# Optimization experiments

Hardware: AMD Instinct MI355X
Metric: run time of the kernel (lower is better)

The kernel has to match this reference:

```python
import jax, jax.numpy as jnp
import numpy as np

N_NODES = 100000
N_EDGES = 1600000
N_GRAPHS = 64


def setup_inputs() -> dict:
    key = jax.random.key(0)
    ks = jax.random.split(key, 12)
    x = jax.random.normal(ks[0], (N_NODES, 3), dtype=jnp.float32)
    edge_index = jax.random.randint(ks[1], (2, N_EDGES), 0, N_NODES)
    edge_attr = jax.random.uniform(ks[2], (N_EDGES,), dtype=jnp.float32)
    batch = jnp.sort(jax.random.randint(ks[3], (N_NODES,), 0, N_GRAPHS))

    def glorot(k, shape):
        lim = float(np.sqrt(6.0 / (shape[0] + shape[1])))
        return jax.random.uniform(k, shape, jnp.float32, -lim, lim)

    W1 = glorot(ks[4], (3, 100));    b1 = jnp.zeros((100,), jnp.float32)
    W2 = glorot(ks[5], (100, 200));  b2 = jnp.zeros((200,), jnp.float32)
    Wl1 = glorot(ks[6], (200, 100)); bl1 = jnp.zeros((100,), jnp.float32)
    Wl2 = glorot(ks[7], (100, 1));   bl2 = jnp.zeros((1,), jnp.float32)
    return {"x": x, "edge_attr": edge_attr, "W1": W1, "b1": b1, "W2": W2,
            "b2": b2, "Wl1": Wl1, "bl1": bl1, "Wl2": Wl2, "bl2": bl2,
            "edge_index": edge_index, "batch": batch}


def gcn_conv(x, edge_index, edge_weight, W, b):
    # PyG GCNConv: linear transform, add self-loops (weight 1), symmetric
    # deg^{-1/2} normalization, scatter-add messages source->target, + bias.
    h = x @ W                                   # [N, out]
    n = h.shape[0]
    loops = jnp.arange(n)
    row = jnp.concatenate([edge_index[0], loops])   # sources
    col = jnp.concatenate([edge_index[1], loops])   # targets
    w = jnp.concatenate([edge_weight, jnp.ones((n,), edge_weight.dtype)])
    deg = jax.ops.segment_sum(w, col, num_segments=n)
    dinv = jnp.where(deg > 0, jax.lax.rsqrt(deg), jnp.zeros_like(deg))
    norm = dinv[row] * w * dinv[col]                # [E+N]
    out = jax.ops.segment_sum(norm[:, None] * h[row], col, num_segments=n)
    return out + b


def reference(x, edge_attr, W1, b1, W2, b2, Wl1, bl1, Wl2, bl2, edge_index, batch):
    h = jax.nn.silu(gcn_conv(x, edge_index, edge_attr, W1, b1))
    h = jax.nn.silu(gcn_conv(h, edge_index, edge_attr, W2, b2))
    # global_mean_pool over graphs in the batch
    sums = jax.ops.segment_sum(h, batch, num_segments=N_GRAPHS)
    counts = jax.ops.segment_sum(jnp.ones((h.shape[0],), h.dtype), batch,
                                 num_segments=N_GRAPHS)
    pooled = sums / jnp.maximum(counts, 1.0)[:, None]   # [G, 200]
    h = jax.nn.silu(pooled @ Wl1 + bl1)
    out = h @ Wl2 + bl2                                  # [G, 1]
    return out.squeeze()
```

## Files before the change

kernel.cpp:

```cpp
#include <hip/hip_runtime.h>

#define NN 100000
#define NE 1600000
#define NG 64
#define CAP 64
#define NPB 80
#define NBUCK 391
#define NBLK 391
#define EPB 4096
#define BCAP 4608
#define NSLOT 32

__device__ __forceinline__ float silu_f(float x) { return x / (1.0f + __expf(-x)); }

__global__ void k_scatter(const int* __restrict__ row, const int* __restrict__ col,
                          const float* __restrict__ ew, int* __restrict__ gcnt,
                          int2* __restrict__ sorted, float* __restrict__ pooled2) {
  __shared__ int h[NBUCK];
  __shared__ int base[NBUCK];
  __shared__ int curh[NBUCK];
  int tid = threadIdx.x;
  for (int i = tid; i < NBUCK; i += 512) { h[i] = 0; curh[i] = 0; }
  for (int i = blockIdx.x * 512 + tid; i < NG * NSLOT * 200; i += NBLK * 512)
    pooled2[i] = 0.0f;
  __syncthreads();
  int s = blockIdx.x * EPB;
  for (int i = 0; i < EPB / 2048; ++i) {
    int e = s + i * 2048 + tid * 4;
    if (e + 3 < NE) {
      int4 c4 = *(const int4*)(col + e);
      atomicAdd(&h[c4.x >> 8], 1);
      atomicAdd(&h[c4.y >> 8], 1);
      atomicAdd(&h[c4.z >> 8], 1);
      atomicAdd(&h[c4.w >> 8], 1);
    } else {
      for (int j = 0; j < 4; ++j) {
        int ee = e + j;
        if (ee < NE) atomicAdd(&h[col[ee] >> 8], 1);
      }
    }
  }
  __syncthreads();
  for (int i = tid; i < NBUCK; i += 512)
    base[i] = (h[i] > 0) ? atomicAdd(&gcnt[i * 16], h[i]) : 0;
  __syncthreads();
  for (int i = 0; i < EPB / 2048; ++i) {
    int e = s + i * 2048 + tid * 4;
    if (e + 3 < NE) {
      int4 r4 = *(const int4*)(row + e);
      int4 c4 = *(const int4*)(col + e);
      float4 w4 = *(const float4*)(ew + e);
#define SC1(cc, rr, ww) { \
  int b = (cc) >> 8; \
  int p = base[b] + atomicAdd(&curh[b], 1); \
  if (p < BCAP) \
    sorted[(size_t)b * BCAP + p] = \
        make_int2((rr) | (((cc) & 255) << 17), __float_as_int(ww)); }
      SC1(c4.x, r4.x, w4.x)
      SC1(c4.y, r4.y, w4.y)
      SC1(c4.z, r4.z, w4.z)
      SC1(c4.w, r4.w, w4.w)
    } else {
      for (int j = 0; j < 4; ++j) {
        int ee = e + j;
        if (ee < NE) { SC1(col[ee], row[ee], ew[ee]) }
      }
#undef SC1
    }
  }
}

__global__ void k_group(const int* __restrict__ gcnt, const int2* __restrict__ sorted,
                        int* __restrict__ cur, int2* __restrict__ buck,
                        float* __restrict__ dinv, const float* __restrict__ x,
                        float* __restrict__ y) {
  __shared__ int cnt[256];
  __shared__ float wsum[256];
  int b = blockIdx.x, tid = threadIdx.x;
  int n = min(gcnt[b * 16], BCAP);
  size_t s = (size_t)b * BCAP;
  if (tid < 256) { cnt[tid] = 0; wsum[tid] = 0.0f; }
  __syncthreads();
  for (int i = tid; i < n; i += 512) {
    int2 pk = sorted[s + i];
    int node = (pk.x >> 17) & 255;
    int rank = atomicAdd(&cnt[node], 1);
    atomicAdd(&wsum[node], __int_as_float(pk.y));
    if (rank < CAP)
      buck[(((size_t)b * 256 + node) << 6) + rank] = make_int2(pk.x & 0x1FFFF, pk.y);
  }
  __syncthreads();
  if (tid < 256) {
    int gnode = b * 256 + tid;
    if (gnode < NN) {
      cur[gnode] = cnt[tid];
      float di = rsqrtf(wsum[tid] + 1.0f);
      dinv[gnode] = di;
      y[3 * gnode + 0] = di * x[3 * gnode + 0];
      y[3 * gnode + 1] = di * x[3 * gnode + 1];
      y[3 * gnode + 2] = di * x[3 * gnode + 2];
    }
  }
}

__global__ void k_agg1z(const int* __restrict__ cur, const int2* __restrict__ buck,
                        const float* __restrict__ dinv, const float* __restrict__ y,
                        const float* __restrict__ W1, const float* __restrict__ b1,
                        float* __restrict__ z1p) {
  int wave = threadIdx.x >> 6, lane = threadIdx.x & 63;
  int sub = lane >> 4, rank = lane & 15;
  int cbase = blockIdx.x * 16 + wave * 4;
  int c = cbase + sub;
  int cnt = min(cur[c], CAP);
  float dc = dinv[c];
  float s0 = 0.0f, s1 = 0.0f, s2 = 0.0f;
  for (int p = rank; p < cnt; p += 16) {
    int2 pk = buck[((size_t)c << 6) + p];
    int r = pk.x;
    float ww = __int_as_float(pk.y);
    s0 += ww * y[3 * r + 0];
    s1 += ww * y[3 * r + 1];
    s2 += ww * y[3 * r + 2];
  }
  for (int s = 8; s; s >>= 1) {
    s0 += __shfl_down(s0, s, 16);
    s1 += __shfl_down(s1, s, 16);
    s2 += __shfl_down(s2, s, 16);
  }
  if (rank == 0) {
    s0 = (s0 + y[3 * c + 0]) * dc;
    s1 = (s1 + y[3 * c + 1]) * dc;
    s2 = (s2 + y[3 * c + 2]) * dc;
  }
  float2 w0, w1, w2, bq;
  if (lane < 50) {
    w0 = ((const float2*)(W1))[lane];
    w1 = ((const float2*)(W1 + 100))[lane];
    w2 = ((const float2*)(W1 + 200))[lane];
    bq = ((const float2*)b1)[lane];
  }
#pragma unroll
  for (int n = 0; n < 4; ++n) {
    float t0 = __shfl(s0, n * 16, 64);
    float t1 = __shfl(s1, n * 16, 64);
    float t2 = __shfl(s2, n * 16, 64);
    float dn = __shfl(dc, n * 16, 64);
    if (lane < 50) {
      float2 o;
      o.x = dn * silu_f(bq.x + t0 * w0.x + t1 * w1.x + t2 * w2.x);
      o.y = dn * silu_f(bq.y + t0 * w0.y + t1 * w1.y + t2 * w2.y);
      ((float2*)(z1p + (size_t)(cbase + n) * 100))[lane] = o;
    }
  }
}

__global__ void k_agg2(const float* __restrict__ z1p, const float* __restrict__ dinv,
                       const int* __restrict__ cur, const int2* __restrict__ buck,
                       float* __restrict__ a2) {
  int wave = threadIdx.x >> 6;
  int lane = threadIdx.x & 63;
  int c = blockIdx.x * 4 + wave;
  if (c >= NN) return;
  int grp = lane >> 5;
  int li = lane & 31;
  bool act = li < 25;
  float dc = dinv[c];
  const float4* zv = (const float4*)z1p;
  float4 acc = make_float4(0.f, 0.f, 0.f, 0.f);
  if (grp == 0 && act) {
    float4 v = zv[(size_t)c * 25 + li];
    acc.x = dc * v.x; acc.y = dc * v.y; acc.z = dc * v.z; acc.w = dc * v.w;
  }
  int cnt = min(cur[c], CAP);
  int2 pk = make_int2(0, 0);
  if (lane < cnt) pk = buck[((size_t)c << 6) + lane];
  int p = 0;
#define GATH(off, rv, cv) \
  int rv = __shfl(pk.x, p + (off) + grp, 64); \
  float cv = __int_as_float(__shfl(pk.y, p + (off) + grp, 64)) * dc;
#define ACC(rv, cv) { \
  float4 v = zv[(size_t)rv * 25 + li]; \
  acc.x += cv * v.x; acc.y += cv * v.y; acc.z += cv * v.z; acc.w += cv * v.w; }
  for (; p + 8 <= cnt; p += 8) {
    GATH(0, r0, c0) GATH(2, r1, c1) GATH(4, r2, c2) GATH(6, r3, c3)
    if (act) { ACC(r0, c0) ACC(r1, c1) ACC(r2, c2) ACC(r3, c3) }
  }
  for (; p + 2 <= cnt; p += 2) {
    GATH(0, r0, c0)
    if (act) ACC(r0, c0)
  }
  if (p < cnt) {
    int r0 = __shfl(pk.x, p, 64);
    float c0 = __int_as_float(__shfl(pk.y, p, 64)) * dc;
    if (grp == 0 && act) ACC(r0, c0)
  }
#undef GATH
#undef ACC
  acc.x += __shfl(acc.x, lane + 32, 64);
  acc.y += __shfl(acc.y, lane + 32, 64);
  acc.z += __shfl(acc.z, lane + 32, 64);
  acc.w += __shfl(acc.w, lane + 32, 64);
  if (grp == 0 && act) ((float4*)a2)[(size_t)c * 25 + li] = acc;
}

__global__ void k_h2pool(const float* __restrict__ a2, const float* __restrict__ W2,
                         const float* __restrict__ b2, const int* __restrict__ batch,
                         float* __restrict__ pooled2) {
  __shared__ float zst[100 * 84];
  __shared__ float part[6 * 200];
  __shared__ int bsm[NPB];
  int tid = threadIdx.x;
  int nb = blockIdx.x * NPB;
  int slot = blockIdx.x & (NSLOT - 1);
  const float4* a2v = (const float4*)(a2 + (size_t)nb * 100);
  for (int i = tid; i < NPB * 25; i += 256) {
    int n = i / 25, c = i % 25;
    float4 v = a2v[i];
    zst[(4 * c + 0) * 84 + n] = v.x;
    zst[(4 * c + 1) * 84 + n] = v.y;
    zst[(4 * c + 2) * 84 + n] = v.z;
    zst[(4 * c + 3) * 84 + n] = v.w;
  }
  if (tid < NPB) bsm[tid] = batch[nb + tid];
  for (int i = tid; i < 1200; i += 256) part[i] = 0.0f;
  __syncthreads();
  int gmin = bsm[0];
  int ngr = bsm[NPB - 1] - gmin + 1;
  int q = tid % 25;
  int r = tid / 25;
  if (r < 10) {
    int n0 = r * 8;
    float4 acc0[8], acc1[8];
#pragma unroll
    for (int i = 0; i < 8; ++i) {
      acc0[i] = make_float4(0.f, 0.f, 0.f, 0.f);
      acc1[i] = make_float4(0.f, 0.f, 0.f, 0.f);
    }
    const float4* W2v = (const float4*)W2;
#pragma unroll 2
    for (int k = 0; k < 100; ++k) {
      float4 w0 = W2v[k * 50 + 2 * q];
      float4 w1 = W2v[k * 50 + 2 * q + 1];
      float4 za = *(const float4*)&zst[k * 84 + n0];
      float4 zb = *(const float4*)&zst[k * 84 + n0 + 4];
#define FMA8(ai, zv) \
  acc0[ai].x += (zv) * w0.x; acc0[ai].y += (zv) * w0.y; \
  acc0[ai].z += (zv) * w0.z; acc0[ai].w += (zv) * w0.w; \
  acc1[ai].x += (zv) * w1.x; acc1[ai].y += (zv) * w1.y; \
  acc1[ai].z += (zv) * w1.z; acc1[ai].w += (zv) * w1.w;
      FMA8(0, za.x) FMA8(1, za.y) FMA8(2, za.z) FMA8(3, za.w)
      FMA8(4, zb.x) FMA8(5, zb.y) FMA8(6, zb.z) FMA8(7, zb.w)
#undef FMA8
    }
    float4 b0v = ((const float4*)b2)[2 * q];
    float4 b1v = ((const float4*)b2)[2 * q + 1];
    float4 run0 = make_float4(0.f, 0.f, 0.f, 0.f);
    float4 run1 = make_float4(0.f, 0.f, 0.f, 0.f);
    int curg = bsm[n0];
#define FLUSH(gv) { \
  int gl = (gv) - gmin; \
  if (gl < 6) { \
    float* pr = &part[gl * 200 + 8 * q]; \
    atomicAdd(&pr[0], run0.x); atomicAdd(&pr[1], run0.y); \
    atomicAdd(&pr[2], run0.z); atomicAdd(&pr[3], run0.w); \
    atomicAdd(&pr[4], run1.x); atomicAdd(&pr[5], run1.y); \
    atomicAdd(&pr[6], run1.z); atomicAdd(&pr[7], run1.w); \
  } else { \
    float* pr = &pooled2[((size_t)(gv) * NSLOT + slot) * 200 + 8 * q]; \
    atomicAdd(&pr[0], run0.x); atomicAdd(&pr[1], run0.y); \
    atomicAdd(&pr[2], run0.z); atomicAdd(&pr[3], run0.w); \
    atomicAdd(&pr[4], run1.x); atomicAdd(&pr[5], run1.y); \
    atomicAdd(&pr[6], run1.z); atomicAdd(&pr[7], run1.w); \
  } }
#pragma unroll
    for (int i = 0; i < 8; ++i) {
      float4 s0, s1;
      s0.x = silu_f(acc0[i].x + b0v.x); s0.y = silu_f(acc0[i].y + b0v.y);
      s0.z = silu_f(acc0[i].z + b0v.z); s0.w = silu_f(acc0[i].w + b0v.w);
      s1.x = silu_f(acc1[i].x + b1v.x); s1.y = silu_f(acc1[i].y + b1v.y);
      s1.z = silu_f(acc1[i].z + b1v.z); s1.w = silu_f(acc1[i].w + b1v.w);
      int g = bsm[n0 + i];
      if (g != curg) {
        FLUSH(curg)
        run0 = make_float4(0.f, 0.f, 0.f, 0.f);
        run1 = make_float4(0.f, 0.f, 0.f, 0.f);
        curg = g;
      }
      run0.x += s0.x; run0.y += s0.y; run0.z += s0.z; run0.w += s0.w;
      run1.x += s1.x; run1.y += s1.y; run1.z += s1.z; run1.w += s1.w;
    }
    FLUSH(curg)
#undef FLUSH
  }
  __syncthreads();
  if (tid < 200) {
    int nloop = min(ngr, 6);
    for (int g = 0; g < nloop; ++g)
      pooled2[((size_t)(gmin + g) * NSLOT + slot) * 200 + tid] = part[g * 200 + tid];
  }
}

__global__ void k_final(const float* __restrict__ pooled2, const int* __restrict__ batch,
                        const float* __restrict__ Wl1, const float* __restrict__ bl1,
                        const float* __restrict__ Wl2, const float* __restrict__ bl2,
                        float* __restrict__ out) {
  __shared__ float pm[200];
  __shared__ float hid[100];
  __shared__ int bounds[2];
  int g = blockIdx.x;
  int j = threadIdx.x;
  if (j < 2) {
    int target = g + j;
    int lo = 0, hi = NN;
    while (lo < hi) {
      int mid = (lo + hi) >> 1;
      if (batch[mid] < target) lo = mid + 1; else hi = mid;
    }
    bounds[j] = lo;
  }
  float acc = 0.0f;
  if (j < 200) {
    const float* base = pooled2 + (size_t)g * NSLOT * 200 + j;
    for (int s = 0; s < NSLOT; ++s) acc += base[s * 200];
  }
  __syncthreads();
  int cntg = bounds[1] - bounds[0];
  float inv = 1.0f / (float)((cntg > 0) ? cntg : 1);
  if (j < 200) pm[j] = acc * inv;
  __syncthreads();
  if (j < 100) {
    float a = bl1[j];
    for (int k = 0; k < 200; ++k) a += pm[k] * Wl1[k * 100 + j];
    a = silu_f(a);
    hid[j] = a * Wl2[j];
  }
  __syncthreads();
  if (j == 0) {
    float sum = bl2[0];
    for (int k = 0; k < 100; ++k) sum += hid[k];
    out[g] = sum;
  }
}

extern "C" void kernel_launch(void* const* d_in, const int* in_sizes, int n_in,
                              void* d_out, int out_size, void* d_ws, size_t ws_size,
                              hipStream_t stream) {
  const float* x   = (const float*)d_in[0];
  const float* ew  = (const float*)d_in[1];
  const float* W1  = (const float*)d_in[2];
  const float* b1  = (const float*)d_in[3];
  const float* W2  = (const float*)d_in[4];
  const float* b2  = (const float*)d_in[5];
  const float* Wl1 = (const float*)d_in[6];
  const float* bl1 = (const float*)d_in[7];
  const float* Wl2 = (const float*)d_in[8];
  const float* bl2 = (const float*)d_in[9];
  const int* ei    = (const int*)d_in[10];
  const int* batch = (const int*)d_in[11];
  const int* rowp = ei;
  const int* colp = ei + NE;
  float* out = (float*)d_out;

  char* w = (char*)d_ws;
  size_t o = 0;
  auto alloc = [&](size_t bytes) {
    char* p = w + o;
    o = (o + bytes + 255) & ~(size_t)255;
    return p;
  };
  int*   cur     = (int*)alloc((size_t)NN * 4);
  float* dinv    = (float*)alloc((size_t)NN * 4);
  float* y       = (float*)alloc((size_t)NN * 3 * 4);
  float* pooled2 = (float*)alloc((size_t)NG * NSLOT * 200 * 4);
  float* z1p     = (float*)alloc((size_t)NN * 100 * 4);
  float* a2      = (float*)alloc((size_t)NN * 100 * 4);
  int2*  buck    = (int2*)alloc((size_t)NN * CAP * 8);
  int2*  sorted  = (int2*)alloc((size_t)NBUCK * BCAP * 8);
  int*   gcnt    = (int*)alloc((size_t)NBUCK * 16 * 4);

  hipMemsetAsync(gcnt, 0, (size_t)NBUCK * 16 * 4, stream);

  k_scatter<<<NBLK, 512, 0, stream>>>(rowp, colp, ew, gcnt, sorted, pooled2);
  k_group<<<NBUCK, 512, 0, stream>>>(gcnt, sorted, cur, buck, dinv, x, y);
  k_agg1z<<<NN / 16, 256, 0, stream>>>(cur, buck, dinv, y, W1, b1, z1p);
  k_agg2<<<(NN + 3) / 4, 256, 0, stream>>>(z1p, dinv, cur, buck, a2);
  k_h2pool<<<NN / NPB, 256, 0, stream>>>(a2, W2, b2, batch, pooled2);
  k_final<<<NG, 256, 0, stream>>>(pooled2, batch, Wl1, bl1, Wl2, bl2, out);
}
```

Before: 340.6 us.

## Recompute layer-1 features per edge from 3-wide aggregates instead of gathering 100-wide rows

Layer-1 output is no longer materialised as a 100-float-per-node array. k_agg1 stores only the normalised 3-component aggregate plus dinv in a float4. k_agg2r then recomputes the W1 transform and silu for each gathered neighbor before accumulating. This replaces the 400-byte-per-edge gathers and the large intermediate write with 16-byte gathers, at the cost of about 100 exponentials and FMAs per edge and the loss of the 8-way unrolled gather loop.

```diff
diff --git a/kernel.cpp b/kernel.cpp
--- a/kernel.cpp
+++ b/kernel.cpp
@@ -72,8 +72,7 @@
 
 __global__ void k_group(const int* __restrict__ gcnt, const int2* __restrict__ sorted,
                         int* __restrict__ cur, int2* __restrict__ buck,
-                        float* __restrict__ dinv, const float* __restrict__ x,
-                        float* __restrict__ y) {
+                        const float* __restrict__ x, float4* __restrict__ y4) {
   __shared__ int cnt[256];
   __shared__ float wsum[256];
   int b = blockIdx.x, tid = threadIdx.x;
@@ -95,32 +94,27 @@
     if (gnode < NN) {
       cur[gnode] = cnt[tid];
       float di = rsqrtf(wsum[tid] + 1.0f);
-      dinv[gnode] = di;
-      y[3 * gnode + 0] = di * x[3 * gnode + 0];
-      y[3 * gnode + 1] = di * x[3 * gnode + 1];
-      y[3 * gnode + 2] = di * x[3 * gnode + 2];
-    }
-  }
-}
-
-__global__ void k_agg1z(const int* __restrict__ cur, const int2* __restrict__ buck,
-                        const float* __restrict__ dinv, const float* __restrict__ y,
-                        const float* __restrict__ W1, const float* __restrict__ b1,
-                        float* __restrict__ z1p) {
+      y4[gnode] = make_float4(di * x[3 * gnode + 0], di * x[3 * gnode + 1],
+                              di * x[3 * gnode + 2], di);
+    }
+  }
+}
+
+__global__ void k_agg1(const int* __restrict__ cur, const int2* __restrict__ buck,
+                       const float4* __restrict__ y4, float4* __restrict__ a1d) {
   int wave = threadIdx.x >> 6, lane = threadIdx.x & 63;
   int sub = lane >> 4, rank = lane & 15;
   int cbase = blockIdx.x * 16 + wave * 4;
   int c = cbase + sub;
   int cnt = min(cur[c], CAP);
-  float dc = dinv[c];
   float s0 = 0.0f, s1 = 0.0f, s2 = 0.0f;
   for (int p = rank; p < cnt; p += 16) {
     int2 pk = buck[((size_t)c << 6) + p];
-    int r = pk.x;
     float ww = __int_as_float(pk.y);
-    s0 += ww * y[3 * r + 0];
-    s1 += ww * y[3 * r + 1];
-    s2 += ww * y[3 * r + 2];
+    float4 v = y4[pk.x];
+    s0 += ww * v.x;
+    s1 += ww * v.y;
+    s2 += ww * v.z;
   }
   for (int s = 8; s; s >>= 1) {
     s0 += __shfl_down(s0, s, 16);
@@ -128,35 +122,15 @@
     s2 += __shfl_down(s2, s, 16);
   }
   if (rank == 0) {
-    s0 = (s0 + y[3 * c + 0]) * dc;
-    s1 = (s1 + y[3 * c + 1]) * dc;
-    s2 = (s2 + y[3 * c + 2]) * dc;
-  }
-  float2 w0, w1, w2, bq;
-  if (lane < 50) {
-    w0 = ((const float2*)(W1))[lane];
-    w1 = ((const float2*)(W1 + 100))[lane];
-    w2 = ((const float2*)(W1 + 200))[lane];
-    bq = ((const float2*)b1)[lane];
-  }
-#pragma unroll
-  for (int n = 0; n < 4; ++n) {
-    float t0 = __shfl(s0, n * 16, 64);
-    float t1 = __shfl(s1, n * 16, 64);
-    float t2 = __shfl(s2, n * 16, 64);
-    float dn = __shfl(dc, n * 16, 64);
-    if (lane < 50) {
-      float2 o;
-      o.x = dn * silu_f(bq.x + t0 * w0.x + t1 * w1.x + t2 * w2.x);
-      o.y = dn * silu_f(bq.y + t0 * w0.y + t1 * w1.y + t2 * w2.y);
-      ((float2*)(z1p + (size_t)(cbase + n) * 100))[lane] = o;
-    }
-  }
-}
-
-__global__ void k_agg2(const float* __restrict__ z1p, const float* __restrict__ dinv,
-                       const int* __restrict__ cur, const int2* __restrict__ buck,
-                       float* __restrict__ a2) {
+    float4 vc = y4[c];
+    float dc = vc.w;
+    a1d[c] = make_float4((s0 + vc.x) * dc, (s1 + vc.y) * dc, (s2 + vc.z) * dc, dc);
+  }
+}
+
+__global__ void k_agg2r(const float4* __restrict__ a1d, const int* __restrict__ cur,
+                        const int2* __restrict__ buck, const float* __restrict__ W1,
+                        const float* __restrict__ b1, float* __restrict__ a2) {
   int wave = threadIdx.x >> 6;
   int lane = threadIdx.x & 63;
   int c = blockIdx.x * 4 + wave;
@@ -164,38 +138,44 @@
   int grp = lane >> 5;
   int li = lane & 31;
   bool act = li < 25;
-  float dc = dinv[c];
-  const float4* zv = (const float4*)z1p;
+  float4 w0, w1, w2, bb;
+  if (act) {
+    w0 = ((const float4*)W1)[li];
+    w1 = ((const float4*)(W1 + 100))[li];
+    w2 = ((const float4*)(W1 + 200))[li];
+    bb = ((const float4*)b1)[li];
+  }
+  float4 ac = a1d[c];
+  float dc = ac.w;
   float4 acc = make_float4(0.f, 0.f, 0.f, 0.f);
-  if (grp == 0 && act) {
-    float4 v = zv[(size_t)c * 25 + li];
-    acc.x = dc * v.x; acc.y = dc * v.y; acc.z = dc * v.z; acc.w = dc * v.w;
-  }
+#define ZACC(av, cf) { \
+  float m = (cf) * (av).w; \
+  float vx = bb.x + (av).x * w0.x + (av).y * w1.x + (av).z * w2.x; \
+  float vy = bb.y + (av).x * w0.y + (av).y * w1.y + (av).z * w2.y; \
+  float vz = bb.z + (av).x * w0.z + (av).y * w1.z + (av).z * w2.z; \
+  float vw = bb.w + (av).x * w0.w + (av).y * w1.w + (av).z * w2.w; \
+  acc.x += m * (vx / (1.0f + __expf(-vx))); \
+  acc.y += m * (vy / (1.0f + __expf(-vy))); \
+  acc.z += m * (vz / (1.0f + __expf(-vz))); \
+  acc.w += m * (vw / (1.0f + __expf(-vw))); }
+  if (grp == 0 && act) ZACC(ac, dc)
   int cnt = min(cur[c], CAP);
   int2 pk = make_int2(0, 0);
   if (lane < cnt) pk = buck[((size_t)c << 6) + lane];
   int p = 0;
-#define GATH(off, rv, cv) \
-  int rv = __shfl(pk.x, p + (off) + grp, 64); \
-  float cv = __int_as_float(__shfl(pk.y, p + (off) + grp, 64)) * dc;
-#define ACC(rv, cv) { \
-  float4 v = zv[(size_t)rv * 25 + li]; \
-  acc.x += cv * v.x; acc.y += cv * v.y; acc.z += cv * v.z; acc.w += cv * v.w; }
-  for (; p + 8 <= cnt; p += 8) {
-    GATH(0, r0, c0) GATH(2, r1, c1) GATH(4, r2, c2) GATH(6, r3, c3)
-    if (act) { ACC(r0, c0) ACC(r1, c1) ACC(r2, c2) ACC(r3, c3) }
-  }
   for (; p + 2 <= cnt; p += 2) {
-    GATH(0, r0, c0)
-    if (act) ACC(r0, c0)
+    int rv = __shfl(pk.x, p + grp, 64);
+    float cf = __int_as_float(__shfl(pk.y, p + grp, 64)) * dc;
+    float4 av = a1d[rv];
+    if (act) ZACC(av, cf)
   }
   if (p < cnt) {
-    int r0 = __shfl(pk.x, p, 64);
-    float c0 = __int_as_float(__shfl(pk.y, p, 64)) * dc;
-    if (grp == 0 && act) ACC(r0, c0)
-  }
-#undef GATH
-#undef ACC
+    int rv = __shfl(pk.x, p, 64);
+    float cf = __int_as_float(__shfl(pk.y, p, 64)) * dc;
+    float4 av = a1d[rv];
+    if (grp == 0 && act) ZACC(av, cf)
+  }
+#undef ZACC
   acc.x += __shfl(acc.x, lane + 32, 64);
   acc.y += __shfl(acc.y, lane + 32, 64);
   acc.z += __shfl(acc.z, lane + 32, 64);
@@ -368,22 +348,21 @@
     o = (o + bytes + 255) & ~(size_t)255;
     return p;
   };
-  int*   cur     = (int*)alloc((size_t)NN * 4);
-  float* dinv    = (float*)alloc((size_t)NN * 4);
-  float* y       = (float*)alloc((size_t)NN * 3 * 4);
-  float* pooled2 = (float*)alloc((size_t)NG * NSLOT * 200 * 4);
-  float* z1p     = (float*)alloc((size_t)NN * 100 * 4);
-  float* a2      = (float*)alloc((size_t)NN * 100 * 4);
-  int2*  buck    = (int2*)alloc((size_t)NN * CAP * 8);
-  int2*  sorted  = (int2*)alloc((size_t)NBUCK * BCAP * 8);
-  int*   gcnt    = (int*)alloc((size_t)NBUCK * 16 * 4);
+  int*    cur     = (int*)alloc((size_t)NN * 4);
+  float4* y4      = (float4*)alloc((size_t)NN * 16);
+  float4* a1d     = (float4*)alloc((size_t)NN * 16);
+  float*  pooled2 = (float*)alloc((size_t)NG * NSLOT * 200 * 4);
+  float*  a2      = (float*)alloc((size_t)NN * 100 * 4);
+  int2*   buck    = (int2*)alloc((size_t)NN * CAP * 8);
+  int2*   sorted  = (int2*)alloc((size_t)NBUCK * BCAP * 8);
+  int*    gcnt    = (int*)alloc((size_t)NBUCK * 16 * 4);
 
   hipMemsetAsync(gcnt, 0, (size_t)NBUCK * 16 * 4, stream);
 
   k_scatter<<<NBLK, 512, 0, stream>>>(rowp, colp, ew, gcnt, sorted, pooled2);
-  k_group<<<NBUCK, 512, 0, stream>>>(gcnt, sorted, cur, buck, dinv, x, y);
-  k_agg1z<<<NN / 16, 256, 0, stream>>>(cur, buck, dinv, y, W1, b1, z1p);
-  k_agg2<<<(NN + 3) / 4, 256, 0, stream>>>(z1p, dinv, cur, buck, a2);
+  k_group<<<NBUCK, 512, 0, stream>>>(gcnt, sorted, cur, buck, x, y4);
+  k_agg1<<<NN / 16, 256, 0, stream>>>(cur, buck, y4, a1d);
+  k_agg2r<<<(NN + 3) / 4, 256, 0, stream>>>(a1d, cur, buck, W1, b1, a2);
   k_h2pool<<<NN / NPB, 256, 0, stream>>>(a2, W2, b2, batch, pooled2);
   k_final<<<NG, 256, 0, stream>>>(pooled2, batch, Wl1, bl1, Wl2, bl2, out);
 }
```

Measured after the change: 334.8 us. About the same (-1.7%).
